# Performance work log

Hardware: AMD Instinct MI355X
Metric: run time of the kernel (lower is better)

## Reference

```python
import jax, jax.numpy as jnp
import numpy as np

N = 12          # microphones
K = 512         # GCC window length (lags)
RES_T = 32      # theta resolution
RES_P = 64      # phi resolution
FS = 16000.0    # sampling frequency
C = 343.0       # speed of sound
B, T = 8, 32    # batch, frames
EPS = 1e-12


def _mic_positions():
    # 5 cm radius uniform circular array in the xy-plane (matches rn init arg)
    ang = 2.0 * np.pi * np.arange(N) / N
    return np.stack([0.05 * np.cos(ang), 0.05 * np.sin(ang), np.zeros(N)], axis=1)


def _compute_tau0():
    """Precompute integer lag indices tau0[n, m, theta, phi] exactly as the torch
    module does (nearest lag on the circular GCC axis), vectorized."""
    theta = np.linspace(0.0, np.pi / 2, RES_T)
    phi = np.linspace(-np.pi, np.pi, RES_P + 1)[:-1]
    # unit direction vectors r: [RES_T, RES_P, 3]
    r = np.stack([np.outer(np.sin(theta), np.cos(phi)),
                  np.outer(np.sin(theta), np.sin(phi)),
                  np.tile(np.cos(theta)[:, None], [1, RES_P])], axis=2)
    rn = _mic_positions()
    diff = rn[None, :, :] - rn[:, None, :]            # [k, l, 3] = rn[l] - rn[k]
    imtdf = np.einsum('tpc,klc->tpkl', r, diff) / C   # TDOA in seconds
    # nearest lag; ceil(x - 0.5) reproduces np.argmin tie-breaking on the
    # tau grid [0..K/2, -K/2+1..-1] (ties go to floor for >0, more-negative for <0)
    lag = np.ceil(imtdf * FS - 0.5).astype(np.int64)
    lag = np.clip(lag, -(K // 2) + 1, K // 2)
    tau0 = lag.transpose(2, 3, 0, 1)                  # [N, N, RES_T, RES_P]
    tau0 = np.where(tau0 < 0, tau0 + K, tau0)         # wrap negative lags (circular GCC)
    return jnp.asarray(tau0, dtype=jnp.int32)


def setup_inputs() -> dict:
    key = jax.random.key(0)
    x = jax.random.normal(key, (B, T, N, N, K), dtype=jnp.float32)
    return {"x": x, "tau0": _compute_tau0()}


def reference(x, tau0):
    # x: [..., N, N, K], tau0: [N, N, RES_T, RES_P]
    lead = x.shape[:-3]
    x2 = x.reshape(lead + (N * N, K))                       # [..., P2, K]
    idx = tau0.reshape(N * N, RES_T * RES_P)                # [P2, G]
    idx_b = jnp.broadcast_to(idx, lead + idx.shape)
    g = jnp.take_along_axis(x2, idx_b, axis=-1)             # [..., P2, G]
    maps = g.sum(axis=-2).reshape(lead + (RES_T, RES_P))    # accumulate over mic pairs
    # normalize: zero-mean over the map, then divide by max (original adds eps first)
    maps = maps - jnp.mean(maps, axis=(-1, -2), keepdims=True) + EPS
    maps = maps / jnp.max(maps, axis=(-1, -2), keepdims=True)
    return maps
```

## Files before the change

### kernel.cpp

```cpp
#include <hip/hip_runtime.h>

#define NPAIR   144
#define KLEN    512
#define GPTS    2048
#define NFRAMES 256
#define STAGE   16
#define EPSV    1e-12f

__global__ void pack_tau_kernel(const int* __restrict__ tau0,
                                unsigned short* __restrict__ tau16, int n) {
    int i = blockIdx.x * 256 + threadIdx.x;
    if (i < n) {
        int pair = i >> 11;
        tau16[i] = (unsigned short)(((pair & (STAGE - 1)) << 9) + tau0[i]);
    }
}

__global__ __launch_bounds__(1024)
void srp_map_kernel(const float* __restrict__ x,
                    const unsigned short* __restrict__ tau16,
                    float* __restrict__ out) {
    __shared__ float rows[STAGE * KLEN];
    __shared__ float red[17];

    const int f = blockIdx.x;
    const int t = threadIdx.x;
    const float* xf = x + (size_t)f * (NPAIR * KLEN);

    float acc0 = 0.0f, acc1 = 0.0f;
    const int g0 = t << 1;

    for (int s = 0; s < NPAIR / STAGE; ++s) {
        const float4* src = (const float4*)(xf + s * (STAGE * KLEN));
        float4* dst = (float4*)rows;
        dst[t]        = src[t];
        dst[t + 1024] = src[t + 1024];
        __syncthreads();

        const unsigned short* tp = tau16 + s * (STAGE * GPTS) + g0;
        #pragma unroll
        for (int p = 0; p < STAGE; ++p) {
            unsigned idx2 = *(const unsigned*)(tp + p * GPTS);
            acc0 += rows[idx2 & 0xffffu];
            acc1 += rows[idx2 >> 16];
        }
        __syncthreads();
    }

    const int wave = t >> 6;
    const int lane = t & 63;

    float sm = acc0 + acc1;
    #pragma unroll
    for (int off = 32; off > 0; off >>= 1) sm += __shfl_down(sm, off, 64);
    if (lane == 0) red[wave] = sm;
    __syncthreads();
    if (t == 0) {
        float tot = 0.0f;
        #pragma unroll
        for (int w = 0; w < 16; ++w) tot += red[w];
        red[16] = tot * (1.0f / (float)GPTS);
    }
    __syncthreads();
    const float mean = red[16];

    const float v0 = acc0 - mean + EPSV;
    const float v1 = acc1 - mean + EPSV;

    float mx = fmaxf(v0, v1);
    #pragma unroll
    for (int off = 32; off > 0; off >>= 1) mx = fmaxf(mx, __shfl_down(mx, off, 64));
    __syncthreads();
    if (lane == 0) red[wave] = mx;
    __syncthreads();
    if (t == 0) {
        float mm = red[0];
        #pragma unroll
        for (int w = 1; w < 16; ++w) mm = fmaxf(mm, red[w]);
        red[16] = mm;
    }
    __syncthreads();
    const float maxv = red[16];

    float2 o;
    o.x = v0 / maxv;
    o.y = v1 / maxv;
    ((float2*)(out + (size_t)f * GPTS))[t] = o;
}

extern "C" void kernel_launch(void* const* d_in, const int* in_sizes, int n_in,
                              void* d_out, int out_size, void* d_ws, size_t ws_size,
                              hipStream_t stream) {
    const float* x    = (const float*)d_in[0];
    const int*   tau0 = (const int*)d_in[1];
    unsigned short* tau16 = (unsigned short*)d_ws;
    float* out = (float*)d_out;

    const int n = NPAIR * GPTS;
    pack_tau_kernel<<<(n + 255) / 256, 256, 0, stream>>>(tau0, tau16, n);
    srp_map_kernel<<<NFRAMES, 1024, 0, stream>>>(x, tau16, out);
}
```

Baseline: 113.0 us.

## Split pair reduction across blocks and gather four frames per float4 lookup

The gather kernel now handles four frames per block, interleaving them in shared memory so each tau index lookup fetches a float4 holding four frames. Each block covers only one eighth of the mic pairs, giving 512 blocks instead of 256. Partial sums are written to workspace, and a separate normalization kernel sums the partials and applies the mean and max normalization. The intent is to reuse tau index loads across frames and use more of the GPU. In exchange it adds a kernel launch and a round trip of partial sums through global memory.

Result: slower. 115.9 us (+2.6%).

```diff
diff --git a/kernel.cpp b/kernel.cpp
--- a/kernel.cpp
+++ b/kernel.cpp
@@ -3,8 +3,13 @@
 #define NPAIR   144
 #define KLEN    512
 #define GPTS    2048
-#define NFRAMES 256
-#define STAGE   16
+#define NFRM    256
+#define FPB     4
+#define NFG     (NFRM / FPB)
+#define NSPLIT  8
+#define PPB     (NPAIR / NSPLIT)
+#define SROWS   6
+#define NSTAGE  (PPB / SROWS)
 #define EPSV    1e-12f
 
 __global__ void pack_tau_kernel(const int* __restrict__ tau0,
@@ -12,80 +17,108 @@
     int i = blockIdx.x * 256 + threadIdx.x;
     if (i < n) {
         int pair = i >> 11;
-        tau16[i] = (unsigned short)(((pair & (STAGE - 1)) << 9) + tau0[i]);
+        tau16[i] = (unsigned short)(((pair % SROWS) << 9) + tau0[i]);
     }
 }
 
 __global__ __launch_bounds__(1024)
-void srp_map_kernel(const float* __restrict__ x,
-                    const unsigned short* __restrict__ tau16,
-                    float* __restrict__ out) {
-    __shared__ float rows[STAGE * KLEN];
-    __shared__ float red[17];
+void srp_gather_kernel(const float* __restrict__ x,
+                       const unsigned short* __restrict__ tau16,
+                       float* __restrict__ part) {
+    __shared__ float4 rows4[SROWS * KLEN];
 
+    const int bi = blockIdx.x;
+    const int sp = bi & (NSPLIT - 1);
+    const int fg = bi >> 3;
+    const int t  = threadIdx.x;
+    const int pair_base = sp * PPB;
+    const float* xg = x + (size_t)(fg * FPB) * NPAIR * KLEN;
+
+    float4 acc0 = {0.f, 0.f, 0.f, 0.f};
+    float4 acc1 = {0.f, 0.f, 0.f, 0.f};
+    const int g0 = t << 1;
+
+    for (int s = 0; s < NSTAGE; ++s) {
+        __syncthreads();
+        if (t < SROWS * 128) {
+            int p  = t >> 7;
+            int k4 = t & 127;
+            const float* src = xg + (size_t)(pair_base + s * SROWS + p) * KLEN + k4 * 4;
+            float4 v0 = *(const float4*)(src);
+            float4 v1 = *(const float4*)(src + 1 * NPAIR * KLEN);
+            float4 v2 = *(const float4*)(src + 2 * NPAIR * KLEN);
+            float4 v3 = *(const float4*)(src + 3 * NPAIR * KLEN);
+            float4* dst = &rows4[p * KLEN + k4 * 4];
+            dst[0] = make_float4(v0.x, v1.x, v2.x, v3.x);
+            dst[1] = make_float4(v0.y, v1.y, v2.y, v3.y);
+            dst[2] = make_float4(v0.z, v1.z, v2.z, v3.z);
+            dst[3] = make_float4(v0.w, v1.w, v2.w, v3.w);
+        }
+        __syncthreads();
+
+        const unsigned short* tp = tau16 + (size_t)(pair_base + s * SROWS) * GPTS + g0;
+        #pragma unroll
+        for (int p = 0; p < SROWS; ++p) {
+            unsigned pk = *(const unsigned*)(tp + (size_t)p * GPTS);
+            float4 v0 = rows4[pk & 0xffffu];
+            float4 v1 = rows4[pk >> 16];
+            acc0.x += v0.x; acc0.y += v0.y; acc0.z += v0.z; acc0.w += v0.w;
+            acc1.x += v1.x; acc1.y += v1.y; acc1.z += v1.z; acc1.w += v1.w;
+        }
+    }
+
+    float* pb = part + ((size_t)sp * NFRM + (size_t)fg * FPB) * GPTS;
+    *(float2*)(pb + 0 * GPTS + g0) = make_float2(acc0.x, acc1.x);
+    *(float2*)(pb + 1 * GPTS + g0) = make_float2(acc0.y, acc1.y);
+    *(float2*)(pb + 2 * GPTS + g0) = make_float2(acc0.z, acc1.z);
+    *(float2*)(pb + 3 * GPTS + g0) = make_float2(acc0.w, acc1.w);
+}
+
+__global__ __launch_bounds__(256)
+void srp_norm_kernel(const float* __restrict__ part, float* __restrict__ out) {
+    __shared__ float red[5];
     const int f = blockIdx.x;
     const int t = threadIdx.x;
-    const float* xf = x + (size_t)f * (NPAIR * KLEN);
 
-    float acc0 = 0.0f, acc1 = 0.0f;
-    const int g0 = t << 1;
-
-    for (int s = 0; s < NPAIR / STAGE; ++s) {
-        const float4* src = (const float4*)(xf + s * (STAGE * KLEN));
-        float4* dst = (float4*)rows;
-        dst[t]        = src[t];
-        dst[t + 1024] = src[t + 1024];
-        __syncthreads();
-
-        const unsigned short* tp = tau16 + s * (STAGE * GPTS) + g0;
-        #pragma unroll
-        for (int p = 0; p < STAGE; ++p) {
-            unsigned idx2 = *(const unsigned*)(tp + p * GPTS);
-            acc0 += rows[idx2 & 0xffffu];
-            acc1 += rows[idx2 >> 16];
-        }
-        __syncthreads();
+    float4 s0 = {0.f, 0.f, 0.f, 0.f};
+    float4 s1 = {0.f, 0.f, 0.f, 0.f};
+    #pragma unroll
+    for (int sp = 0; sp < NSPLIT; ++sp) {
+        const float4* p = (const float4*)(part + ((size_t)sp * NFRM + f) * GPTS);
+        float4 a = p[t], b = p[t + 256];
+        s0.x += a.x; s0.y += a.y; s0.z += a.z; s0.w += a.w;
+        s1.x += b.x; s1.y += b.y; s1.z += b.z; s1.w += b.w;
     }
 
-    const int wave = t >> 6;
-    const int lane = t & 63;
+    const int wave = t >> 6, lane = t & 63;
 
-    float sm = acc0 + acc1;
+    float sm = s0.x + s0.y + s0.z + s0.w + s1.x + s1.y + s1.z + s1.w;
     #pragma unroll
     for (int off = 32; off > 0; off >>= 1) sm += __shfl_down(sm, off, 64);
     if (lane == 0) red[wave] = sm;
     __syncthreads();
-    if (t == 0) {
-        float tot = 0.0f;
-        #pragma unroll
-        for (int w = 0; w < 16; ++w) tot += red[w];
-        red[16] = tot * (1.0f / (float)GPTS);
-    }
+    if (t == 0) red[4] = (red[0] + red[1] + red[2] + red[3]) * (1.0f / (float)GPTS);
     __syncthreads();
-    const float mean = red[16];
+    const float mean = red[4];
 
-    const float v0 = acc0 - mean + EPSV;
-    const float v1 = acc1 - mean + EPSV;
+    s0.x = s0.x - mean + EPSV; s0.y = s0.y - mean + EPSV;
+    s0.z = s0.z - mean + EPSV; s0.w = s0.w - mean + EPSV;
+    s1.x = s1.x - mean + EPSV; s1.y = s1.y - mean + EPSV;
+    s1.z = s1.z - mean + EPSV; s1.w = s1.w - mean + EPSV;
 
-    float mx = fmaxf(v0, v1);
+    float mx = fmaxf(fmaxf(fmaxf(s0.x, s0.y), fmaxf(s0.z, s0.w)),
+                     fmaxf(fmaxf(s1.x, s1.y), fmaxf(s1.z, s1.w)));
     #pragma unroll
     for (int off = 32; off > 0; off >>= 1) mx = fmaxf(mx, __shfl_down(mx, off, 64));
-    __syncthreads();
     if (lane == 0) red[wave] = mx;
     __syncthreads();
-    if (t == 0) {
-        float mm = red[0];
-        #pragma unroll
-        for (int w = 1; w < 16; ++w) mm = fmaxf(mm, red[w]);
-        red[16] = mm;
-    }
+    if (t == 0) red[4] = fmaxf(fmaxf(red[0], red[1]), fmaxf(red[2], red[3]));
     __syncthreads();
-    const float maxv = red[16];
+    const float inv = 1.0f / red[4];
 
-    float2 o;
-    o.x = v0 / maxv;
-    o.y = v1 / maxv;
-    ((float2*)(out + (size_t)f * GPTS))[t] = o;
+    float4* o = (float4*)(out + (size_t)f * GPTS);
+    o[t]       = make_float4(s0.x * inv, s0.y * inv, s0.z * inv, s0.w * inv);
+    o[t + 256] = make_float4(s1.x * inv, s1.y * inv, s1.z * inv, s1.w * inv);
 }
 
 extern "C" void kernel_launch(void* const* d_in, const int* in_sizes, int n_in,
@@ -93,10 +126,13 @@
                               hipStream_t stream) {
     const float* x    = (const float*)d_in[0];
     const int*   tau0 = (const int*)d_in[1];
+    float* out = (float*)d_out;
+
     unsigned short* tau16 = (unsigned short*)d_ws;
-    float* out = (float*)d_out;
+    float* part = (float*)((char*)d_ws + (1 << 20));
 
     const int n = NPAIR * GPTS;
     pack_tau_kernel<<<(n + 255) / 256, 256, 0, stream>>>(tau0, tau16, n);
-    srp_map_kernel<<<NFRAMES, 1024, 0, stream>>>(x, tau16, out);
+    srp_gather_kernel<<<NFG * NSPLIT, 1024, 0, stream>>>(x, tau16, part);
+    srp_norm_kernel<<<NFRM, 256, 0, stream>>>(part, out);
 }
```
